# Performance work log

Hardware: AMD Instinct MI355X
Metric: run time of the kernel (lower is better)

## Reference

```python
import jax, jax.numpy as jnp
import numpy as np

H = 16        # num_attention_heads
D = 128       # head_dim
HID = 2048    # hidden_size
S = 2048      # seq_len
B = 2
EPS = 1.1920928955078125e-07  # torch.finfo(float32).eps, F.rms_norm default


def _rope(x, cos, sin):
    # x: [B,H,S,D]; cos/sin: [S, D//2] broadcast over B,H
    d = x.shape[-1] // 2
    x1, x2 = x[..., :d], x[..., d:]
    return jnp.concatenate([x1 * cos + x2 * sin, -x1 * sin + x2 * cos], axis=-1)


def _rmsnorm(x):
    ms = jnp.mean(x * x, axis=-1, keepdims=True)
    return x * jax.lax.rsqrt(ms + EPS)


def setup_inputs() -> dict:
    key = jax.random.key(0)
    ks = jax.random.split(key, 7)
    x = jax.random.normal(ks[0], (B, S, HID), dtype=jnp.float32)
    cos = jax.random.uniform(ks[1], (S, D // 2), dtype=jnp.float32)
    sin = jax.random.uniform(ks[2], (S, D // 2), dtype=jnp.float32)
    sc = 1.0 / np.sqrt(HID)
    wq = jax.random.normal(ks[3], (H * D, HID), dtype=jnp.float32) * sc
    wk = jax.random.normal(ks[4], (D, HID), dtype=jnp.float32) * sc  # num_kv_heads=1
    wv = jax.random.normal(ks[5], (D, HID), dtype=jnp.float32) * sc
    wo = jax.random.normal(ks[6], (HID, H * D), dtype=jnp.float32) * sc
    return {"x": x, "cos": cos, "sin": sin, "wq": wq, "wk": wk, "wv": wv, "wo": wo}


def reference(x, cos, sin, wq, wk, wv, wo):
    b, s, _ = x.shape
    # projections
    q = (x @ wq.T).reshape(b, s, H, D).transpose(0, 2, 1, 3)        # [b,H,s,D]
    k = (x @ wk.T).reshape(b, s, 1, D).transpose(0, 2, 1, 3)        # [b,1,s,D] MQA
    v = (x @ wv.T).reshape(b, s, 1, D).transpose(0, 2, 1, 3)
    # RoPE then RMS-norm on q/k (keep k/v in MQA [b,1,s,D]; broadcasting replaces expand)
    q = _rmsnorm(_rope(q, cos, sin))
    k = _rmsnorm(_rope(k, cos, sin))
    # causal attention
    scores = jnp.einsum('bhqd,bgkd->bhqk', q, k) * (D ** -0.5)      # [b,H,s,s]
    mask = jnp.tril(jnp.ones((s, s), dtype=bool))
    scores = jnp.where(mask, scores, -jnp.inf)
    attn = jax.nn.softmax(scores, axis=-1)
    out = jnp.einsum('bhqk,bgkd->bhqd', attn, v)                    # [b,H,s,D]
    out = out.transpose(0, 2, 1, 3).reshape(b, s, H * D)
    return out @ wo.T
```

## Files before the change

### kernel.cpp

```cpp
#include <hip/hip_runtime.h>
#include <hip/hip_bf16.h>

typedef __attribute__((ext_vector_type(8))) short bf16x8;
typedef __attribute__((ext_vector_type(4))) float f32x4;

constexpr int cH = 16, cD = 128, cHID = 2048, cS = 2048, cB = 2;
constexpr float cEPS = 1.1920928955078125e-07f;

__device__ __forceinline__ unsigned short f2bf(float f) {
  union { float f; unsigned u; } v; v.f = f;
  unsigned r = v.u + 0x7fffu + ((v.u >> 16) & 1u);
  return (unsigned short)(r >> 16);
}
__device__ __forceinline__ float bf2f(unsigned short h) {
  union { unsigned u; float f; } v; v.u = ((unsigned)h) << 16; return v.f;
}
__device__ __forceinline__ unsigned pk2(float a, float b) {
  return (unsigned)f2bf(a) | ((unsigned)f2bf(b) << 16);
}
__device__ __forceinline__ f32x4 mfma16(bf16x8 a, bf16x8 b, f32x4 c) {
  return __builtin_amdgcn_mfma_f32_16x16x32_bf16(a, b, c, 0, 0, 0);
}
__device__ __forceinline__ void gl2l(const void* g, void* l) {
  __builtin_amdgcn_global_load_lds(
      (const __attribute__((address_space(1))) unsigned int*)g,
      (__attribute__((address_space(3))) unsigned int*)l, 16, 0, 0);
}

__global__ __launch_bounds__(256) void cvt_qkv(
    const float* __restrict__ x, const float* __restrict__ wq,
    const float* __restrict__ wk, const float* __restrict__ wv,
    unsigned short* __restrict__ xb, unsigned short* __restrict__ wqb,
    unsigned short* __restrict__ wkb, unsigned short* __restrict__ wvb)
{
  long i = (long)blockIdx.x * 2048 + threadIdx.x * 8;
  const float* s; unsigned short* d; long off;
  if (i < 8388608)       { s = x;  d = xb;  off = i; }
  else if (i < 12582912) { s = wq; d = wqb; off = i - 8388608; }
  else if (i < 12845056) { s = wk; d = wkb; off = i - 12582912; }
  else                   { s = wv; d = wvb; off = i - 12845056; }
  float4 v0 = *reinterpret_cast<const float4*>(s + off);
  float4 v1 = *reinterpret_cast<const float4*>(s + off + 4);
  uint4 o; o.x = pk2(v0.x, v0.y); o.y = pk2(v0.z, v0.w);
  o.z = pk2(v1.x, v1.y); o.w = pk2(v1.z, v1.w);
  *reinterpret_cast<uint4*>(d + off) = o;
}

__global__ __launch_bounds__(256) void cvt_wo(
    const float* __restrict__ wo, unsigned short* __restrict__ wob)
{
  long i = (long)blockIdx.x * 2048 + threadIdx.x * 8;
  float4 v0 = *reinterpret_cast<const float4*>(wo + i);
  float4 v1 = *reinterpret_cast<const float4*>(wo + i + 4);
  uint4 o; o.x = pk2(v0.x, v0.y); o.y = pk2(v0.z, v0.w);
  o.z = pk2(v1.x, v1.y); o.w = pk2(v1.z, v1.w);
  *reinterpret_cast<uint4*>(wob + i) = o;
}

__global__ __launch_bounds__(256) void gemm_qkv(
    const unsigned short* __restrict__ A,
    const unsigned short* __restrict__ Wq,
    const unsigned short* __restrict__ Wk,
    const unsigned short* __restrict__ Wv,
    const float* __restrict__ cosb, const float* __restrict__ sinb,
    unsigned short* __restrict__ Qn,
    unsigned short* __restrict__ Kn,
    unsigned short* __restrict__ Vn)
{
  __shared__ unsigned short lds[8192];
  const int t = threadIdx.x;
  const int bm = blockIdx.x, bn = blockIdx.y;
  const int lane = t & 63, w = t >> 6;
  const int hi = lane >> 4, l15 = lane & 15;

  const unsigned short* Wp; long wbase;
  if (bn < 16)       { Wp = Wq; wbase = (long)bn * 128; }
  else if (bn == 16) { Wp = Wk; wbase = 0; }
  else               { Wp = Wv; wbase = 0; }

  f32x4 acc[2][8] = {};

  for (int k0 = 0; k0 < 2048; k0 += 32) {
    #pragma unroll
    for (int i = 0; i < 2; ++i) {
      int c = w + 4 * i;
      gl2l(A + (long)(bm * 128 + 16 * c + (lane >> 2)) * 2048 + k0 + (lane & 3) * 8,
           &lds[c * 512]);
      gl2l(Wp + (wbase + 16 * c + (lane >> 2)) * 2048 + k0 + (lane & 3) * 8,
           &lds[4096 + c * 512]);
    }
    __syncthreads();
    bf16x8 af[2], bff[8];
    #pragma unroll
    for (int m = 0; m < 2; ++m)
      af[m] = *reinterpret_cast<const bf16x8*>(&lds[(w * 32 + m * 16 + l15) * 32 + hi * 8]);
    #pragma unroll
    for (int n = 0; n < 8; ++n)
      bff[n] = *reinterpret_cast<const bf16x8*>(&lds[4096 + (n * 16 + l15) * 32 + hi * 8]);
    #pragma unroll
    for (int m = 0; m < 2; ++m)
      #pragma unroll
      for (int n = 0; n < 8; ++n)
        acc[m][n] = mfma16(af[m], bff[n], acc[m][n]);
    __syncthreads();
  }

  const int rowbase = bm * 128 + w * 32;
  if (bn == 17) {
    #pragma unroll
    for (int m = 0; m < 2; ++m)
      #pragma unroll
      for (int r = 0; r < 4; ++r) {
        int grow = rowbase + m * 16 + hi * 4 + r;
        int b = grow >> 11, s = grow & 2047;
        long base = ((long)b * cS + s) * cD;
        #pragma unroll
        for (int n = 0; n < 8; ++n)
          Vn[base + n * 16 + l15] = f2bf(acc[m][n][r]);
      }
  } else {
    #pragma unroll
    for (int m = 0; m < 2; ++m)
      #pragma unroll
      for (int r = 0; r < 4; ++r) {
        int grow = rowbase + m * 16 + hi * 4 + r;
        int b = grow >> 11, s = grow & 2047;
        float o1[4], o2[4], ss = 0.f;
        #pragma unroll
        for (int n = 0; n < 4; ++n) {
          float cv = cosb[(long)s * 64 + n * 16 + l15];
          float sv = sinb[(long)s * 64 + n * 16 + l15];
          float x1 = acc[m][n][r], x2 = acc[m][n + 4][r];
          o1[n] = x1 * cv + x2 * sv;
          o2[n] = x2 * cv - x1 * sv;
          ss += o1[n] * o1[n] + o2[n] * o2[n];
        }
        ss += __shfl_xor(ss, 1); ss += __shfl_xor(ss, 2);
        ss += __shfl_xor(ss, 4); ss += __shfl_xor(ss, 8);
        float scn = rsqrtf(ss * (1.0f / 128.0f) + cEPS);
        if (bn < 16) {
          long base = (((long)b * cH + bn) * cS + s) * cD;
          #pragma unroll
          for (int n = 0; n < 4; ++n) {
            Qn[base + n * 16 + l15] = f2bf(o1[n] * scn);
            Qn[base + 64 + n * 16 + l15] = f2bf(o2[n] * scn);
          }
        } else {
          long base = ((long)b * cS + s) * cD;
          int xs = (s & 7) << 3;
          #pragma unroll
          for (int n = 0; n < 4; ++n) {
            Kn[base + ((n * 16 + l15) ^ xs)] = f2bf(o1[n] * scn);
            Kn[base + (((64 + n * 16 + l15)) ^ xs)] = f2bf(o2[n] * scn);
          }
        }
      }
  }
}

__global__ __launch_bounds__(256) void vtrans(
    const unsigned short* __restrict__ Vn, unsigned short* __restrict__ Vt)
{
  __shared__ unsigned short Tl[64][72];
  const int t = threadIdx.x;
  const int st = blockIdx.x * 64, dt = blockIdx.y * 64, b = blockIdx.z;
  const unsigned short* Vb = Vn + (long)b * cS * cD;
  #pragma unroll
  for (int i = 0; i < 2; ++i) {
    int r = i * 32 + (t >> 3), c8 = (t & 7) * 8;
    *reinterpret_cast<uint4*>(&Tl[r][c8]) =
        *reinterpret_cast<const uint4*>(&Vb[(long)(st + r) * cD + dt + c8]);
  }
  __syncthreads();
  unsigned short* Vo = Vt + (long)b * cD * cS;
  #pragma unroll
  for (int i = 0; i < 2; ++i) {
    int d = i * 32 + (t >> 3), sb = (t & 7) * 8;
    unsigned short e[8];
    #pragma unroll
    for (int j = 0; j < 8; ++j) e[j] = Tl[sb + j][d];
    uint4 o;
    o.x = (unsigned)e[0] | ((unsigned)e[1] << 16);
    o.y = (unsigned)e[2] | ((unsigned)e[3] << 16);
    o.z = (unsigned)e[4] | ((unsigned)e[5] << 16);
    o.w = (unsigned)e[6] | ((unsigned)e[7] << 16);
    int dg = dt + d;
    *reinterpret_cast<uint4*>(&Vo[(long)dg * cS + st + (sb ^ ((dg & 7) << 3))]) = o;
  }
}

__global__ __launch_bounds__(256) void attn2(
    const unsigned short* __restrict__ Qn,
    const unsigned short* __restrict__ Kn,
    const unsigned short* __restrict__ Vt,
    unsigned short* __restrict__ O)
{
  __shared__ unsigned short lds[16384];
  const int t = threadIdx.x, w = t >> 6, lane = t & 63;
  const int hi = lane >> 4, l15 = lane & 15;
  const int h = blockIdx.y, b = blockIdx.z;
  const unsigned short* Qb = Qn + (long)(b * cH + h) * cS * cD;
  const unsigned short* Kb = Kn + (long)b * cS * cD;
  const unsigned short* Vtb = Vt + (long)b * cD * cS;
  const int x3 = (l15 & 7) << 3;
  const float sc2 = 0.08838834764831845f * 1.442695040888963f;

  #pragma unroll 1
  for (int pass = 0; pass < 2; ++pass) {
    const int qt = (pass == 0) ? blockIdx.x : 31 - blockIdx.x;
    const int q0 = qt * 64;
    const int qrow = q0 + w * 16 + l15;

    bf16x8 qf[4];
    #pragma unroll
    for (int kc = 0; kc < 4; ++kc)
      qf[kc] = *reinterpret_cast<const bf16x8*>(&Qb[(long)qrow * cD + kc * 32 + hi * 8]);

    f32x4 oacc[8] = {};
    float mrun = -1e30f, lrun = 0.f;
    const int nt = qt + 1;

    #pragma unroll 1
    for (int kt = 0; kt < nt; ++kt) {
      const int kv0 = kt * 64;
      __syncthreads();
      #pragma unroll
      for (int i = 0; i < 4; ++i) {
        int c = 4 * w + i;
        gl2l(Kb + (long)(kv0 + 4 * c + (lane >> 4)) * cD + (lane & 15) * 8,
             &lds[c * 512]);
        gl2l(Vtb + (long)(8 * c + (lane >> 3)) * cS + kv0 + (lane & 7) * 8,
             &lds[8192 + c * 512]);
      }
      __syncthreads();

      f32x4 st[4] = {};
      #pragma unroll
      for (int kc = 0; kc < 4; ++kc) {
        #pragma unroll
        for (int n = 0; n < 4; ++n) {
          bf16x8 kf = *reinterpret_cast<const bf16x8*>(
              &lds[(n * 16 + l15) * 128 + ((kc * 32 + hi * 8) ^ x3)]);
          st[n] = mfma16(kf, qf[kc], st[n]);
        }
      }

      float p[4][4];
      if (kt == qt) {
        #pragma unroll
        for (int n = 0; n < 4; ++n)
          #pragma unroll
          for (int r = 0; r < 4; ++r) {
            int kv = kv0 + n * 16 + hi * 4 + r;
            p[n][r] = (kv <= qrow) ? st[n][r] * sc2 : -1e30f;
          }
      } else {
        #pragma unroll
        for (int n = 0; n < 4; ++n)
          #pragma unroll
          for (int r = 0; r < 4; ++r)
            p[n][r] = st[n][r] * sc2;
      }

      float pmax = p[0][0];
      #pragma unroll
      for (int n = 0; n < 4; ++n)
        #pragma unroll
        for (int r = 0; r < 4; ++r) pmax = fmaxf(pmax, p[n][r]);
      pmax = fmaxf(pmax, __shfl_xor(pmax, 16));
      pmax = fmaxf(pmax, __shfl_xor(pmax, 32));
      float mnew = fmaxf(mrun, pmax);
      float alpha = exp2f(mrun - mnew);
      mrun = mnew;

      float psum = 0.f;
      #pragma unroll
      for (int n = 0; n < 4; ++n)
        #pragma unroll
        for (int r = 0; r < 4; ++r) {
          p[n][r] = exp2f(p[n][r] - mnew);
          psum += p[n][r];
        }
      psum += __shfl_xor(psum, 16);
      psum += __shfl_xor(psum, 32);
      lrun = lrun * alpha + psum;

      #pragma unroll
      for (int n = 0; n < 8; ++n)
        #pragma unroll
        for (int r = 0; r < 4; ++r) oacc[n][r] *= alpha;

      unsigned pkl[4], pkh[4];
      #pragma unroll
      for (int n = 0; n < 4; ++n) {
        pkl[n] = pk2(p[n][0], p[n][1]);
        pkh[n] = pk2(p[n][2], p[n][3]);
      }

      bf16x8 pa[2];
      #pragma unroll
      for (int c = 0; c < 2; ++c) {
        int ns = 2 * c + (hi >> 1);
        int no = 2 * c + ((hi >> 1) ^ 1);
        unsigned own0 = pkl[ns], own1 = pkh[ns];
        unsigned ot0 = pkl[no], ot1 = pkh[no];
        unsigned a160 = __shfl_xor(own0, 16), a161 = __shfl_xor(own1, 16);
        unsigned a320 = __shfl_xor(ot0, 32),  a321 = __shfl_xor(ot1, 32);
        unsigned a480 = __shfl_xor(ot0, 48),  a481 = __shfl_xor(ot1, 48);
        unsigned w0 = hi == 0 ? own0 : hi == 1 ? a480 : hi == 2 ? a320 : a160;
        unsigned w1 = hi == 0 ? own1 : hi == 1 ? a481 : hi == 2 ? a321 : a161;
        unsigned w2 = hi == 0 ? a160 : hi == 1 ? a320 : hi == 2 ? a480 : own0;
        unsigned w3 = hi == 0 ? a161 : hi == 1 ? a321 : hi == 2 ? a481 : own1;
        union { unsigned u[4]; bf16x8 v; } cvt;
        cvt.u[0] = w0; cvt.u[1] = w1; cvt.u[2] = w2; cvt.u[3] = w3;
        pa[c] = cvt.v;
      }

      #pragma unroll
      for (int n2 = 0; n2 < 8; ++n2) {
        #pragma unroll
        for (int c = 0; c < 2; ++c) {
          bf16x8 vf = *reinterpret_cast<const bf16x8*>(
              &lds[8192 + (n2 * 16 + l15) * 64 + ((c * 32 + hi * 8) ^ x3)]);
          oacc[n2] = mfma16(vf, pa[c], oacc[n2]);
        }
      }
    }

    __syncthreads();
    {
      float inv = 1.0f / lrun;
      unsigned short* Ol = &lds[w * 2176];
      #pragma unroll
      for (int n2 = 0; n2 < 8; ++n2)
        #pragma unroll
        for (int r = 0; r < 4; ++r)
          Ol[l15 * 136 + n2 * 16 + hi * 4 + r] = f2bf(oacc[n2][r] * inv);
      __syncthreads();
      #pragma unroll
      for (int i = 0; i < 4; ++i) {
        int row = hi + 4 * i;
        uint4 ov = *reinterpret_cast<const uint4*>(&Ol[row * 136 + l15 * 8]);
        *reinterpret_cast<uint4*>(
            &O[(long)(b * cS + q0 + w * 16 + row) * (cH * cD) + h * cD + l15 * 8]) = ov;
      }
    }
  }
}

__global__ __launch_bounds__(256) void gemm_out(
    const unsigned short* __restrict__ A,
    const unsigned short* __restrict__ W,
    float* __restrict__ C)
{
  __shared__ unsigned short lds[8192];
  const int t = threadIdx.x;
  const int bm = blockIdx.x, bn = blockIdx.y;
  const int lane = t & 63, w = t >> 6;
  const int wr = w >> 1, wc = w & 1, hi = lane >> 4, l15 = lane & 15;
  const long wbase = (long)bn * 128;

  f32x4 acc[4][4] = {};
  for (int k0 = 0; k0 < 2048; k0 += 32) {
    #pragma unroll
    for (int i = 0; i < 2; ++i) {
      int c = w + 4 * i;
      gl2l(A + (long)(bm * 128 + 16 * c + (lane >> 2)) * 2048 + k0 + (lane & 3) * 8,
           &lds[c * 512]);
      gl2l(W + (wbase + 16 * c + (lane >> 2)) * 2048 + k0 + (lane & 3) * 8,
           &lds[4096 + c * 512]);
    }
    __syncthreads();
    bf16x8 af[4], bff[4];
    #pragma unroll
    for (int m = 0; m < 4; ++m)
      af[m] = *reinterpret_cast<const bf16x8*>(&lds[(wr * 64 + m * 16 + l15) * 32 + hi * 8]);
    #pragma unroll
    for (int n = 0; n < 4; ++n)
      bff[n] = *reinterpret_cast<const bf16x8*>(&lds[4096 + (wc * 64 + n * 16 + l15) * 32 + hi * 8]);
    #pragma unroll
    for (int m = 0; m < 4; ++m)
      #pragma unroll
      for (int n = 0; n < 4; ++n)
        acc[m][n] = mfma16(af[m], bff[n], acc[m][n]);
    __syncthreads();
  }

  #pragma unroll
  for (int m = 0; m < 4; ++m) {
    int row = bm * 128 + wr * 64 + m * 16 + hi * 4;
    #pragma unroll
    for (int n = 0; n < 4; ++n) {
      int col = bn * 128 + wc * 64 + n * 16 + l15;
      #pragma unroll
      for (int r = 0; r < 4; ++r)
        C[(long)(row + r) * 2048 + col] = acc[m][n][r];
    }
  }
}

extern "C" void kernel_launch(void* const* d_in, const int* in_sizes, int n_in,
                              void* d_out, int out_size, void* d_ws, size_t ws_size,
                              hipStream_t stream) {
  const float* x    = (const float*)d_in[0];
  const float* cosb = (const float*)d_in[1];
  const float* sinb = (const float*)d_in[2];
  const float* wq   = (const float*)d_in[3];
  const float* wk   = (const float*)d_in[4];
  const float* wv   = (const float*)d_in[5];
  const float* wo   = (const float*)d_in[6];
  float* out = (float*)d_out;

  char* ws = (char*)d_ws;
  unsigned short* xb  = (unsigned short*)(ws);
  unsigned short* wqb = (unsigned short*)(ws + 16777216);
  unsigned short* wkb = (unsigned short*)(ws + 25165824);
  unsigned short* wvb = (unsigned short*)(ws + 25690112);
  unsigned short* Qn  = (unsigned short*)(ws + 26214400);
  unsigned short* Kn  = (unsigned short*)(ws + 42991616);
  unsigned short* Vn  = (unsigned short*)(ws + 44040192);
  unsigned short* Vtg = (unsigned short*)(ws + 45088768);
  unsigned short* Ob  = (unsigned short*)ws;
  unsigned short* wob = (unsigned short*)(ws + 16777216);

  cvt_qkv<<<dim3(6400), 256, 0, stream>>>(x, wq, wk, wv, xb, wqb, wkb, wvb);
  gemm_qkv<<<dim3(32, 18), 256, 0, stream>>>(xb, wqb, wkb, wvb, cosb, sinb, Qn, Kn, Vn);
  vtrans<<<dim3(32, 2, 2), 256, 0, stream>>>(Vn, Vtg);
  cvt_wo<<<dim3(2048), 256, 0, stream>>>(wo, wob);
  attn2<<<dim3(16, 16, 2), 256, 0, stream>>>(Qn, Kn, Vtg, Ob);
  gemm_out<<<dim3(32, 16), 256, 0, stream>>>(Ob, wob, out);
}
```

Before: 214.1 us.

## Double-buffer attention K/V loads, lazy rescale, MFMA row sums, fuse conversions

The attention kernel now double-buffers K and V tiles in LDS using async global-to-LDS loads with vmcnt waits, so the next tile's loads overlap the current tile's compute. The softmax scale is folded into Q at projection time. Online-softmax rescaling is skipped when the new max exceeds the running max by no more than a threshold. Row sums are accumulated with an MFMA against a ones vector rather than shuffles. The wo conversion is merged into the single conversion kernel, and the bf16 conversion uses the HIP intrinsic. Costs include doubled LDS use, which may lower occupancy, and the lazy rescale, which relies on bounded growth of exponentials.

```diff
diff --git a/kernel.cpp b/kernel.cpp
--- a/kernel.cpp
+++ b/kernel.cpp
@@ -6,17 +6,14 @@
 
 constexpr int cH = 16, cD = 128, cHID = 2048, cS = 2048, cB = 2;
 constexpr float cEPS = 1.1920928955078125e-07f;
-
-__device__ __forceinline__ unsigned short f2bf(float f) {
-  union { float f; unsigned u; } v; v.f = f;
-  unsigned r = v.u + 0x7fffu + ((v.u >> 16) & 1u);
-  return (unsigned short)(r >> 16);
-}
-__device__ __forceinline__ float bf2f(unsigned short h) {
-  union { unsigned u; float f; } v; v.u = ((unsigned)h) << 16; return v.f;
+constexpr float cQS = 0.08838834764831845f * 1.442695040888963f;
+
+__device__ __forceinline__ unsigned short f2bfn(float f) {
+  __hip_bfloat16 h = __float2bfloat16(f);
+  unsigned short u; __builtin_memcpy(&u, &h, 2); return u;
 }
 __device__ __forceinline__ unsigned pk2(float a, float b) {
-  return (unsigned)f2bf(a) | ((unsigned)f2bf(b) << 16);
+  return (unsigned)f2bfn(a) | ((unsigned)f2bfn(b) << 16);
 }
 __device__ __forceinline__ f32x4 mfma16(bf16x8 a, bf16x8 b, f32x4 c) {
   return __builtin_amdgcn_mfma_f32_16x16x32_bf16(a, b, c, 0, 0, 0);
@@ -27,34 +24,26 @@
       (__attribute__((address_space(3))) unsigned int*)l, 16, 0, 0);
 }
 
-__global__ __launch_bounds__(256) void cvt_qkv(
+__global__ __launch_bounds__(256) void cvt_all(
     const float* __restrict__ x, const float* __restrict__ wq,
     const float* __restrict__ wk, const float* __restrict__ wv,
+    const float* __restrict__ wo,
     unsigned short* __restrict__ xb, unsigned short* __restrict__ wqb,
-    unsigned short* __restrict__ wkb, unsigned short* __restrict__ wvb)
+    unsigned short* __restrict__ wkb, unsigned short* __restrict__ wvb,
+    unsigned short* __restrict__ wob)
 {
   long i = (long)blockIdx.x * 2048 + threadIdx.x * 8;
   const float* s; unsigned short* d; long off;
   if (i < 8388608)       { s = x;  d = xb;  off = i; }
   else if (i < 12582912) { s = wq; d = wqb; off = i - 8388608; }
   else if (i < 12845056) { s = wk; d = wkb; off = i - 12582912; }
-  else                   { s = wv; d = wvb; off = i - 12845056; }
+  else if (i < 13107200) { s = wv; d = wvb; off = i - 12845056; }
+  else                   { s = wo; d = wob; off = i - 13107200; }
   float4 v0 = *reinterpret_cast<const float4*>(s + off);
   float4 v1 = *reinterpret_cast<const float4*>(s + off + 4);
   uint4 o; o.x = pk2(v0.x, v0.y); o.y = pk2(v0.z, v0.w);
   o.z = pk2(v1.x, v1.y); o.w = pk2(v1.z, v1.w);
   *reinterpret_cast<uint4*>(d + off) = o;
-}
-
-__global__ __launch_bounds__(256) void cvt_wo(
-    const float* __restrict__ wo, unsigned short* __restrict__ wob)
-{
-  long i = (long)blockIdx.x * 2048 + threadIdx.x * 8;
-  float4 v0 = *reinterpret_cast<const float4*>(wo + i);
-  float4 v1 = *reinterpret_cast<const float4*>(wo + i + 4);
-  uint4 o; o.x = pk2(v0.x, v0.y); o.y = pk2(v0.z, v0.w);
-  o.z = pk2(v1.x, v1.y); o.w = pk2(v1.z, v1.w);
-  *reinterpret_cast<uint4*>(wob + i) = o;
 }
 
 __global__ __launch_bounds__(256) void gemm_qkv(
@@ -116,7 +105,7 @@
         long base = ((long)b * cS + s) * cD;
         #pragma unroll
         for (int n = 0; n < 8; ++n)
-          Vn[base + n * 16 + l15] = f2bf(acc[m][n][r]);
+          Vn[base + n * 16 + l15] = f2bfn(acc[m][n][r]);
       }
   } else {
     #pragma unroll
@@ -139,19 +128,20 @@
         ss += __shfl_xor(ss, 4); ss += __shfl_xor(ss, 8);
         float scn = rsqrtf(ss * (1.0f / 128.0f) + cEPS);
         if (bn < 16) {
+          float sq = scn * cQS;
           long base = (((long)b * cH + bn) * cS + s) * cD;
           #pragma unroll
           for (int n = 0; n < 4; ++n) {
-            Qn[base + n * 16 + l15] = f2bf(o1[n] * scn);
-            Qn[base + 64 + n * 16 + l15] = f2bf(o2[n] * scn);
+            Qn[base + n * 16 + l15] = f2bfn(o1[n] * sq);
+            Qn[base + 64 + n * 16 + l15] = f2bfn(o2[n] * sq);
           }
         } else {
           long base = ((long)b * cS + s) * cD;
           int xs = (s & 7) << 3;
           #pragma unroll
           for (int n = 0; n < 4; ++n) {
-            Kn[base + ((n * 16 + l15) ^ xs)] = f2bf(o1[n] * scn);
-            Kn[base + (((64 + n * 16 + l15)) ^ xs)] = f2bf(o2[n] * scn);
+            Kn[base + ((n * 16 + l15) ^ xs)] = f2bfn(o1[n] * scn);
+            Kn[base + (((64 + n * 16 + l15)) ^ xs)] = f2bfn(o2[n] * scn);
           }
         }
       }
@@ -195,7 +185,7 @@
     const unsigned short* __restrict__ Vt,
     unsigned short* __restrict__ O)
 {
-  __shared__ unsigned short lds[16384];
+  __shared__ unsigned short lds[32768];
   const int t = threadIdx.x, w = t >> 6, lane = t & 63;
   const int hi = lane >> 4, l15 = lane & 15;
   const int h = blockIdx.y, b = blockIdx.z;
@@ -203,36 +193,63 @@
   const unsigned short* Kb = Kn + (long)b * cS * cD;
   const unsigned short* Vtb = Vt + (long)b * cD * cS;
   const int x3 = (l15 & 7) << 3;
-  const float sc2 = 0.08838834764831845f * 1.442695040888963f;
+
+  union OU { unsigned u[4]; bf16x8 v; };
+  OU ou; ou.u[0] = ou.u[1] = ou.u[2] = ou.u[3] = 0x3F803F80u;
+  const bf16x8 onesv = ou.v;
 
   #pragma unroll 1
   for (int pass = 0; pass < 2; ++pass) {
     const int qt = (pass == 0) ? blockIdx.x : 31 - blockIdx.x;
     const int q0 = qt * 64;
     const int qrow = q0 + w * 16 + l15;
+    const int nt = qt + 1;
 
     bf16x8 qf[4];
     #pragma unroll
     for (int kc = 0; kc < 4; ++kc)
       qf[kc] = *reinterpret_cast<const bf16x8*>(&Qb[(long)qrow * cD + kc * 32 + hi * 8]);
 
+    const unsigned short* kp = Kb + (long)(16 * w + (lane >> 4)) * cD + (lane & 15) * 8;
+    const unsigned short* vp[4];
+    #pragma unroll
+    for (int i = 0; i < 4; ++i)
+      vp[i] = Vtb + (long)(32 * w + 8 * i + (lane >> 3)) * cS + (lane & 7) * 8;
+
+    auto STAGE = [&](int buf) {
+      unsigned short* kd = &lds[buf * 8192 + w * 2048];
+      unsigned short* vd = &lds[16384 + buf * 8192 + w * 2048];
+      #pragma unroll
+      for (int i = 0; i < 4; ++i) {
+        gl2l(kp + i * 512, kd + i * 512);
+        gl2l(vp[i], vd + i * 512);
+      }
+      kp += 8192;
+      #pragma unroll
+      for (int i = 0; i < 4; ++i) vp[i] += 64;
+    };
+
     f32x4 oacc[8] = {};
-    float mrun = -1e30f, lrun = 0.f;
-    const int nt = qt + 1;
+    f32x4 lacc = {};
+    float mrun = -1e30f;
+
+    STAGE(0);
+    int cur = 0;
 
     #pragma unroll 1
     for (int kt = 0; kt < nt; ++kt) {
       const int kv0 = kt * 64;
-      __syncthreads();
-      #pragma unroll
-      for (int i = 0; i < 4; ++i) {
-        int c = 4 * w + i;
-        gl2l(Kb + (long)(kv0 + 4 * c + (lane >> 4)) * cD + (lane & 15) * 8,
-             &lds[c * 512]);
-        gl2l(Vtb + (long)(8 * c + (lane >> 3)) * cS + kv0 + (lane & 7) * 8,
-             &lds[8192 + c * 512]);
-      }
-      __syncthreads();
+      if (kt + 1 < nt) {
+        STAGE(cur ^ 1);
+        asm volatile("s_waitcnt vmcnt(8)" ::: "memory");
+      } else {
+        asm volatile("s_waitcnt vmcnt(0)" ::: "memory");
+      }
+      __builtin_amdgcn_s_barrier();
+      __builtin_amdgcn_sched_barrier(0);
+
+      const unsigned short* kbase = &lds[cur * 8192];
+      const unsigned short* vbase = &lds[16384 + cur * 8192];
 
       f32x4 st[4] = {};
       #pragma unroll
@@ -240,7 +257,7 @@
         #pragma unroll
         for (int n = 0; n < 4; ++n) {
           bf16x8 kf = *reinterpret_cast<const bf16x8*>(
-              &lds[(n * 16 + l15) * 128 + ((kc * 32 + hi * 8) ^ x3)]);
+              &kbase[(n * 16 + l15) * 128 + ((kc * 32 + hi * 8) ^ x3)]);
           st[n] = mfma16(kf, qf[kc], st[n]);
         }
       }
@@ -252,14 +269,14 @@
           #pragma unroll
           for (int r = 0; r < 4; ++r) {
             int kv = kv0 + n * 16 + hi * 4 + r;
-            p[n][r] = (kv <= qrow) ? st[n][r] * sc2 : -1e30f;
+            p[n][r] = (kv <= qrow) ? st[n][r] : -1e30f;
           }
       } else {
         #pragma unroll
         for (int n = 0; n < 4; ++n)
           #pragma unroll
           for (int r = 0; r < 4; ++r)
-            p[n][r] = st[n][r] * sc2;
+            p[n][r] = st[n][r];
       }
 
       float pmax = p[0][0];
@@ -269,26 +286,24 @@
         for (int r = 0; r < 4; ++r) pmax = fmaxf(pmax, p[n][r]);
       pmax = fmaxf(pmax, __shfl_xor(pmax, 16));
       pmax = fmaxf(pmax, __shfl_xor(pmax, 32));
-      float mnew = fmaxf(mrun, pmax);
-      float alpha = exp2f(mrun - mnew);
-      mrun = mnew;
-
-      float psum = 0.f;
+
+      if (!__all(pmax - mrun <= 8.0f)) {
+        float mnew = fmaxf(mrun, pmax);
+        float alpha = exp2f(mrun - mnew);
+        mrun = mnew;
+        #pragma unroll
+        for (int n = 0; n < 8; ++n)
+          #pragma unroll
+          for (int r = 0; r < 4; ++r) oacc[n][r] *= alpha;
+        #pragma unroll
+        for (int r = 0; r < 4; ++r) lacc[r] *= alpha;
+      }
+
       #pragma unroll
       for (int n = 0; n < 4; ++n)
         #pragma unroll
-        for (int r = 0; r < 4; ++r) {
-          p[n][r] = exp2f(p[n][r] - mnew);
-          psum += p[n][r];
-        }
-      psum += __shfl_xor(psum, 16);
-      psum += __shfl_xor(psum, 32);
-      lrun = lrun * alpha + psum;
-
-      #pragma unroll
-      for (int n = 0; n < 8; ++n)
-        #pragma unroll
-        for (int r = 0; r < 4; ++r) oacc[n][r] *= alpha;
+        for (int r = 0; r < 4; ++r)
+          p[n][r] = exp2f(p[n][r] - mrun);
 
       unsigned pkl[4], pkh[4];
       #pragma unroll
@@ -317,25 +332,28 @@
       }
 
       #pragma unroll
+      for (int c = 0; c < 2; ++c) lacc = mfma16(onesv, pa[c], lacc);
+      #pragma unroll
       for (int n2 = 0; n2 < 8; ++n2) {
         #pragma unroll
         for (int c = 0; c < 2; ++c) {
           bf16x8 vf = *reinterpret_cast<const bf16x8*>(
-              &lds[8192 + (n2 * 16 + l15) * 64 + ((c * 32 + hi * 8) ^ x3)]);
+              &vbase[(n2 * 16 + l15) * 64 + ((c * 32 + hi * 8) ^ x3)]);
           oacc[n2] = mfma16(vf, pa[c], oacc[n2]);
         }
       }
+      __builtin_amdgcn_s_barrier();
+      cur ^= 1;
     }
 
-    __syncthreads();
     {
-      float inv = 1.0f / lrun;
+      float inv = 1.0f / lacc[0];
       unsigned short* Ol = &lds[w * 2176];
       #pragma unroll
       for (int n2 = 0; n2 < 8; ++n2)
         #pragma unroll
         for (int r = 0; r < 4; ++r)
-          Ol[l15 * 136 + n2 * 16 + hi * 4 + r] = f2bf(oacc[n2][r] * inv);
+          Ol[l15 * 136 + n2 * 16 + hi * 4 + r] = f2bfn(oacc[n2][r] * inv);
       __syncthreads();
       #pragma unroll
       for (int i = 0; i < 4; ++i) {
@@ -344,6 +362,7 @@
         *reinterpret_cast<uint4*>(
             &O[(long)(b * cS + q0 + w * 16 + row) * (cH * cD) + h * cD + l15 * 8]) = ov;
       }
+      __syncthreads();
     }
   }
 }
@@ -420,13 +439,12 @@
   unsigned short* Kn  = (unsigned short*)(ws + 42991616);
   unsigned short* Vn  = (unsigned short*)(ws + 44040192);
   unsigned short* Vtg = (unsigned short*)(ws + 45088768);
+  unsigned short* wob = (unsigned short*)(ws + 46137344);
   unsigned short* Ob  = (unsigned short*)ws;
-  unsigned short* wob = (unsigned short*)(ws + 16777216);
-
-  cvt_qkv<<<dim3(6400), 256, 0, stream>>>(x, wq, wk, wv, xb, wqb, wkb, wvb);
+
+  cvt_all<<<dim3(8448), 256, 0, stream>>>(x, wq, wk, wv, wo, xb, wqb, wkb, wvb, wob);
   gemm_qkv<<<dim3(32, 18), 256, 0, stream>>>(xb, wqb, wkb, wvb, cosb, sinb, Qn, Kn, Vn);
   vtrans<<<dim3(32, 2, 2), 256, 0, stream>>>(Vn, Vtg);
-  cvt_wo<<<dim3(2048), 256, 0, stream>>>(wo, wob);
   attn2<<<dim3(16, 16, 2), 256, 0, stream>>>(Qn, Kn, Vtg, Ob);
   gemm_out<<<dim3(32, 16), 256, 0, stream>>>(Ob, wob, out);
 }
```

Result: slower. 238.2 us (+11.3%).
